# Kernel tuning notes

Hardware: AMD Instinct MI355X
Metric: run time of the kernel (lower is better)

## Reference

```python
import jax, jax.numpy as jnp
import numpy as np

H = 16
D_MODEL = 1024
D_K = D_MODEL // H
B, S = 2, 2048


def setup_inputs() -> dict:
    key = jax.random.key(0)
    ks = jax.random.split(key, 11)
    scale = 1.0 / np.sqrt(D_MODEL)
    inp = {
        "query": jax.random.normal(ks[0], (B, S, D_MODEL), jnp.float32),
        "key": jax.random.normal(ks[1], (B, S, D_MODEL), jnp.float32),
        "value": jax.random.normal(ks[2], (B, S, D_MODEL), jnp.float32),
        # four nn.Linear(d_model, d_model): Wq, Wk, Wv, Wo (torch convention: y = x @ W.T + b)
        "Wq": jax.random.uniform(ks[3], (D_MODEL, D_MODEL), jnp.float32, -scale, scale),
        "bq": jax.random.uniform(ks[4], (D_MODEL,), jnp.float32, -scale, scale),
        "Wk": jax.random.uniform(ks[5], (D_MODEL, D_MODEL), jnp.float32, -scale, scale),
        "bk": jax.random.uniform(ks[6], (D_MODEL,), jnp.float32, -scale, scale),
        "Wv": jax.random.uniform(ks[7], (D_MODEL, D_MODEL), jnp.float32, -scale, scale),
        "bv": jax.random.uniform(ks[8], (D_MODEL,), jnp.float32, -scale, scale),
        "Wo": jax.random.uniform(ks[9], (D_MODEL, D_MODEL), jnp.float32, -scale, scale),
        "bo": jax.random.uniform(ks[10], (D_MODEL,), jnp.float32, -scale, scale),
    }
    return inp


def _split_heads(x):
    # [B, S, D] -> [B, H, S, d_k]
    b, s, _ = x.shape
    return x.reshape(b, s, H, D_K).transpose(0, 2, 1, 3)


def reference(query, key, value, Wq, bq, Wk, bk, Wv, bv, Wo, bo):
    q = _split_heads(query @ Wq.T + bq)
    k = _split_heads(key @ Wk.T + bk)
    v = _split_heads(value @ Wv.T + bv)
    # scaled dot-product attention (dropout omitted: reference is eval-mode)
    scores = jnp.einsum("bhqd,bhkd->bhqk", q, k) / np.sqrt(D_K).astype(np.float32)
    p = jax.nn.softmax(scores, axis=-1)
    x = jnp.einsum("bhqk,bhkd->bhqd", p, v)
    x = x.transpose(0, 2, 1, 3).reshape(query.shape[0], -1, H * D_K)
    return x @ Wo.T + bo
```

## Files before the change

kernel.cpp:

```cpp
#include <hip/hip_runtime.h>

typedef unsigned short u16;
typedef unsigned int u32;
typedef __attribute__((ext_vector_type(8))) short short8;
typedef __attribute__((ext_vector_type(4))) float floatx4;
typedef __attribute__((ext_vector_type(4))) unsigned short ushortx4;
typedef __attribute__((ext_vector_type(4))) unsigned int uint4v;

#define DEV static __device__ __forceinline__

DEV float bf2f(u16 u) { union { unsigned u; float f; } v; v.u = ((unsigned)u) << 16; return v.f; }
DEV u16 f2bf(float f) {
  union { float f; unsigned u; } v; v.f = f;
  return (u16)((v.u + 0x7FFFu + ((v.u >> 16) & 1u)) >> 16);
}
DEV u32 pkbf(float a, float b) {
  union { float f; u32 u; } x, y; x.f = a; y.f = b;
  return __builtin_amdgcn_perm(y.u + 0x8000u, x.u + 0x8000u, 0x07060302u);
}
DEV float fexp2(float x) { return __builtin_amdgcn_exp2f(x); }

#define GLDS(g, l) __builtin_amdgcn_global_load_lds( \
    (const __attribute__((address_space(1))) void*)(g), \
    (__attribute__((address_space(3))) void*)(l), 16, 0, 0)

struct CvtArg {
  const float* src[11];
  u16* dst[11];
  int cum[12];
};

__global__ void convert(CvtArg a) {
  const long base = ((long)blockIdx.x * 256 + threadIdx.x) * 4;
  if (base >= a.cum[11]) return;
  int s = 0;
  while (s < 10 && base >= a.cum[s + 1]) ++s;
  const long off = base - a.cum[s];
  const float* sp = a.src[s] + off;
  ushortx4 u;
#pragma unroll
  for (int r = 0; r < 4; ++r) u[r] = f2bf(sp[r]);
  *(ushortx4*)(a.dst[s] + off) = u;
}

struct GemmArg {
  const u16* x;
  const u16* w;
  const u16* bias;
  u16* dst;
  int mode;
};

__global__ __launch_bounds__(256, 2) void gemm_nt(GemmArg g0, GemmArg g1, GemmArg g2) {
  GemmArg g = (blockIdx.z == 0) ? g0 : ((blockIdx.z == 1) ? g1 : g2);
  __shared__ u16 As[128 * 32];
  __shared__ u16 Bs[128 * 32];
  const int tid = threadIdx.x, w = tid >> 6, l = tid & 63;
  const int l15 = l & 15, quad = l >> 4;
  const int bm = blockIdx.x, bn = blockIdx.y;
  const int wm = w >> 1, wn = w & 1;

  floatx4 acc[4][4];
#pragma unroll
  for (int i = 0; i < 4; ++i)
#pragma unroll
    for (int j = 0; j < 4; ++j) acc[i][j] = (floatx4){0.f, 0.f, 0.f, 0.f};

  const u16* xb = g.x + (long)(bm * 128 + w * 16 + (l >> 2)) * 1024 + (l & 3) * 8;
  const u16* wb = g.w + (long)(bn * 128 + w * 16 + (l >> 2)) * 1024 + (l & 3) * 8;
  u16* asb = &As[(w * 16) * 32];
  u16* bsb = &Bs[(w * 16) * 32];

  for (int kt = 0; kt < 32; ++kt) {
    const int k0 = kt * 32;
    __syncthreads();
#pragma unroll
    for (int p = 0; p < 2; ++p) {
      GLDS(xb + (long)p * 64 * 1024 + k0, asb + p * 64 * 32);
      GLDS(wb + (long)p * 64 * 1024 + k0, bsb + p * 64 * 32);
    }
    __syncthreads();
    short8 af[4], bfr[4];
#pragma unroll
    for (int mi = 0; mi < 4; ++mi)
      af[mi] = *(const short8*)&As[(wm * 64 + mi * 16 + l15) * 32 + quad * 8];
#pragma unroll
    for (int ni = 0; ni < 4; ++ni)
      bfr[ni] = *(const short8*)&Bs[(wn * 64 + ni * 16 + l15) * 32 + quad * 8];
#pragma unroll
    for (int mi = 0; mi < 4; ++mi)
#pragma unroll
      for (int ni = 0; ni < 4; ++ni)
        acc[mi][ni] = __builtin_amdgcn_mfma_f32_16x16x32_bf16(af[mi], bfr[ni], acc[mi][ni], 0, 0, 0);
  }

  float bv[4];
#pragma unroll
  for (int ni = 0; ni < 4; ++ni) bv[ni] = bf2f(g.bias[bn * 128 + wn * 64 + ni * 16 + l15]);

#pragma unroll
  for (int mi = 0; mi < 4; ++mi) {
    const int mbase = bm * 128 + wm * 64 + mi * 16 + quad * 4;
#pragma unroll
    for (int ni = 0; ni < 4; ++ni) {
      const int n = bn * 128 + wn * 64 + ni * 16 + l15;
      if (g.mode == 2) {
        const int b = mbase >> 11, s = mbase & 2047;
        const int h = n >> 6, d = n & 63;
        ushortx4 u;
#pragma unroll
        for (int r = 0; r < 4; ++r) u[r] = f2bf(acc[mi][ni][r] + bv[ni]);
        *(ushortx4*)&g.dst[((long)(b * 16 + h) * 64 + d) * 2048 + s] = u;
      } else if (g.mode == 3) {
        float* df = (float*)g.dst;
#pragma unroll
        for (int r = 0; r < 4; ++r)
          df[(long)(mbase + r) * 1024 + n] = acc[mi][ni][r] + bv[ni];
      } else {
        const float sc = (g.mode == 0) ? 0.18033688011f : 1.0f;
        const int h = n >> 6, d = n & 63;
#pragma unroll
        for (int r = 0; r < 4; ++r) {
          const int m = mbase + r, b = m >> 11, s = m & 2047;
          g.dst[((long)(b * 16 + h) * 2048 + s) * 64 + d] = f2bf((acc[mi][ni][r] + bv[ni]) * sc);
        }
      }
    }
  }
}

__global__ __launch_bounds__(256, 2) void attn_flash(const u16* __restrict__ Q,
                                                     const u16* __restrict__ K,
                                                     const u16* __restrict__ V,
                                                     u16* __restrict__ X) {
  __shared__ u16 Ks[2][64 * 72];
  const int tid = threadIdx.x, w = tid >> 6, l = tid & 63;
  const int l15 = l & 15, quad = l >> 4;

  const int bid = blockIdx.x;
  const int xcd = bid & 7, idx = bid >> 3;
  const int qx = idx & 15, bh = xcd + 8 * (idx >> 4);
  const int q0 = qx * 128;

  const u16* qp = Q + (long)bh * 2048 * 64;
  const u16* kp = K + (long)bh * 2048 * 64;
  const u16* vp = V + (long)bh * 2048 * 64;

  const int r0 = tid >> 3, c0 = tid & 7, r1 = 32 + (tid >> 3);

#define ISSUE_K(kv0) \
    sk0 = *(const short8*)(kp + (long)((kv0) + r0) * 64 + c0 * 8); \
    sk1 = *(const short8*)(kp + (long)((kv0) + r1) * 64 + c0 * 8);

#define STORE_K(pb_) \
    *(short8*)&Ks[pb_][r0 * 72 + c0 * 8] = sk0; \
    *(short8*)&Ks[pb_][r1 * 72 + c0 * 8] = sk1;

  short8 sk0, sk1;

  short8 qf[2][2];
#pragma unroll
  for (int nq = 0; nq < 2; ++nq)
#pragma unroll
    for (int kc = 0; kc < 2; ++kc)
      qf[nq][kc] = *(const short8*)(qp + (long)(q0 + w * 32 + nq * 16 + l15) * 64 + kc * 32 + quad * 8);

  floatx4 o[2][4];
#pragma unroll
  for (int nq = 0; nq < 2; ++nq)
#pragma unroll
    for (int nd = 0; nd < 4; ++nd) o[nq][nd] = (floatx4){0.f, 0.f, 0.f, 0.f};
  float den[2] = {0.f, 0.f};

  const bool p1 = (l & 32) != 0;
  const bool p3 = (l & 16) != 0;
  const bool p2 = p1 ^ p3;

#define BFLY(pbv, m00, m01, m10, m11) { \
    u32 A0 = p1 ? (m10) : (m00), A1 = p1 ? (m11) : (m01); \
    u32 s0_ = p1 ? (m00) : (m10), s1_ = p1 ? (m01) : (m11); \
    u32 B0 = (u32)__shfl_xor((int)s0_, 32), B1 = (u32)__shfl_xor((int)s1_, 32); \
    u32 t0 = p2 ? A0 : B0, t1 = p2 ? A1 : B1; \
    u32 u0 = (u32)__shfl_xor((int)t0, 16), u1 = (u32)__shfl_xor((int)t1, 16); \
    u32 w0 = p2 ? B0 : A0, w1 = p2 ? B1 : A1; \
    pbv[0] = p3 ? u0 : w0; pbv[1] = p3 ? u1 : w1; \
    pbv[2] = p3 ? w0 : u0; pbv[3] = p3 ? w1 : u1; \
  }

  ISSUE_K(0)
  STORE_K(0)
  ISSUE_K(64)
  __syncthreads();

  for (int t = 0; t < 32; ++t) {
    const int p = t & 1;

    short8 vf[2][4];
#pragma unroll
    for (int kc = 0; kc < 2; ++kc)
#pragma unroll
      for (int nd = 0; nd < 4; ++nd)
        vf[kc][nd] = *(const short8*)(vp + (long)(nd * 16 + l15) * 2048 + (long)t * 64 + kc * 32 + quad * 8);

    u32 pk[2][4][2];
#pragma unroll
    for (int mk = 0; mk < 4; ++mk) {
      short8 ak0 = *(const short8*)&Ks[p][(mk * 16 + l15) * 72 + quad * 8];
      short8 ak1 = *(const short8*)&Ks[p][(mk * 16 + l15) * 72 + 32 + quad * 8];
#pragma unroll
      for (int nq = 0; nq < 2; ++nq) {
        floatx4 st = (floatx4){0.f, 0.f, 0.f, 0.f};
        st = __builtin_amdgcn_mfma_f32_16x16x32_bf16(ak0, qf[nq][0], st, 0, 0, 0);
        st = __builtin_amdgcn_mfma_f32_16x16x32_bf16(ak1, qf[nq][1], st, 0, 0, 0);
        const float e0 = fexp2(st[0]), e1 = fexp2(st[1]);
        const float e2 = fexp2(st[2]), e3 = fexp2(st[3]);
        den[nq] += (e0 + e1) + (e2 + e3);
        pk[nq][mk][0] = pkbf(e0, e1);
        pk[nq][mk][1] = pkbf(e2, e3);
      }
    }

#pragma unroll
    for (int kc = 0; kc < 2; ++kc) {
#pragma unroll
      for (int nq = 0; nq < 2; ++nq) {
        uint4v pb;
        BFLY(pb, pk[nq][2 * kc][0], pk[nq][2 * kc][1], pk[nq][2 * kc + 1][0], pk[nq][2 * kc + 1][1])
        short8 pbs = __builtin_bit_cast(short8, pb);
#pragma unroll
        for (int nd = 0; nd < 4; ++nd)
          o[nq][nd] = __builtin_amdgcn_mfma_f32_16x16x32_bf16(vf[kc][nd], pbs, o[nq][nd], 0, 0, 0);
      }
    }

    if (t < 31) {
      STORE_K(p ^ 1)
      if (t < 30) {
        ISSUE_K((t + 2) * 64)
      }
    }
    __syncthreads();
  }

  float rcp[2];
#pragma unroll
  for (int nq = 0; nq < 2; ++nq) {
    float d = den[nq];
    d += __shfl_xor(d, 16);
    d += __shfl_xor(d, 32);
    rcp[nq] = 1.0f / d;
  }

  const int b = bh >> 4, h = bh & 15;
#pragma unroll
  for (int nq = 0; nq < 2; ++nq) {
    const int s = q0 + w * 32 + nq * 16 + l15;
    u16* xrow = X + ((long)(b * 2048 + s)) * 1024 + h * 64;
#pragma unroll
    for (int nd = 0; nd < 4; ++nd) {
      ushortx4 u;
#pragma unroll
      for (int r = 0; r < 4; ++r) u[r] = f2bf(o[nq][nd][r] * rcp[nq]);
      *(ushortx4*)&xrow[nd * 16 + quad * 4] = u;
    }
  }
}

extern "C" void kernel_launch(void* const* d_in, const int* in_sizes, int n_in,
                              void* d_out, int out_size, void* d_ws, size_t ws_size,
                              hipStream_t stream) {
  u16* ws = (u16*)d_ws;
  const size_t M1 = 1048576, M4 = 4194304;
  u16* NQ  = ws;
  u16* NK  = ws + M4;
  u16* NV  = ws + 2 * M4;
  u16* NWQ = ws + 3 * M4;
  u16* NWK = ws + 3 * M4 + M1;
  u16* NWV = ws + 3 * M4 + 2 * M1;
  u16* NWO = ws + 3 * M4 + 3 * M1;
  u16* NBQ = ws + 3 * M4 + 4 * M1;
  u16* NBK = NBQ + 1024;
  u16* NBV = NBQ + 2048;
  u16* NBO = NBQ + 3072;
  u16* Qb = ws + 16 * M1 + 8192;
  u16* Kb = Qb + M4;
  u16* Vb = Qb + 2 * M4;
  u16* Xb = NQ;

  CvtArg ca;
  u16* dsts[11] = {NQ, NK, NV, NWQ, NBQ, NWK, NBK, NWV, NBV, NWO, NBO};
  int sizes[11] = {(int)M4, (int)M4, (int)M4, (int)M1, 1024, (int)M1, 1024, (int)M1, 1024, (int)M1, 1024};
  int c = 0;
  for (int i = 0; i < 11; ++i) {
    ca.src[i] = (const float*)d_in[i];
    ca.dst[i] = dsts[i];
    ca.cum[i] = c;
    c += sizes[i];
  }
  ca.cum[11] = c;
  convert<<<(c / 4 + 255) / 256, 256, 0, stream>>>(ca);

  GemmArg gq{NQ, NWQ, NBQ, Qb, 0};
  GemmArg gk{NK, NWK, NBK, Kb, 1};
  GemmArg gv{NV, NWV, NBV, Vb, 2};
  gemm_nt<<<dim3(32, 8, 3), 256, 0, stream>>>(gq, gk, gv);

  attn_flash<<<dim3(512), 256, 0, stream>>>(Qb, Kb, Vb, Xb);

  GemmArg go{Xb, NWO, NBO, (u16*)d_out, 3};
  gemm_nt<<<dim3(32, 8, 1), 256, 0, stream>>>(go, go, go);
}
```

Baseline: 244.3 us.

## Split KV tile across waves, stage V in LDS, use fp16 for PV

Flash attention now stages V tiles in shared memory alongside K with a double buffer, instead of each wave reading V directly from global memory. Work is re-partitioned so each wave handles 64 query rows against half of each 64-key tile. The two key-halves are merged at the end through shared memory. V and the probabilities switch to fp16 with a pack-with-truncation conversion and an f16 MFMA for the PV product. This is meant to cut redundant global V loads and the bf16 rounding overhead, at the cost of more registers per wave, an extra cross-wave reduction, and fp16 range and precision risk on V.

New measurement: 228.4 us. 1.07x faster.

```diff
diff --git a/kernel.cpp b/kernel.cpp
--- a/kernel.cpp
+++ b/kernel.cpp
@@ -3,6 +3,7 @@
 typedef unsigned short u16;
 typedef unsigned int u32;
 typedef __attribute__((ext_vector_type(8))) short short8;
+typedef __attribute__((ext_vector_type(8))) _Float16 half8;
 typedef __attribute__((ext_vector_type(4))) float floatx4;
 typedef __attribute__((ext_vector_type(4))) unsigned short ushortx4;
 typedef __attribute__((ext_vector_type(4))) unsigned int uint4v;
@@ -14,9 +15,9 @@
   union { float f; unsigned u; } v; v.f = f;
   return (u16)((v.u + 0x7FFFu + ((v.u >> 16) & 1u)) >> 16);
 }
-DEV u32 pkbf(float a, float b) {
-  union { float f; u32 u; } x, y; x.f = a; y.f = b;
-  return __builtin_amdgcn_perm(y.u + 0x8000u, x.u + 0x8000u, 0x07060302u);
+DEV u16 f2h(float f) { return __builtin_bit_cast(u16, (_Float16)f); }
+DEV u32 pkh(float a, float b) {
+  return __builtin_bit_cast(u32, __builtin_amdgcn_cvt_pkrtz(a, b));
 }
 DEV float fexp2(float x) { return __builtin_amdgcn_exp2f(x); }
 
@@ -109,7 +110,7 @@
         const int h = n >> 6, d = n & 63;
         ushortx4 u;
 #pragma unroll
-        for (int r = 0; r < 4; ++r) u[r] = f2bf(acc[mi][ni][r] + bv[ni]);
+        for (int r = 0; r < 4; ++r) u[r] = f2h(acc[mi][ni][r] + bv[ni]);
         *(ushortx4*)&g.dst[((long)(b * 16 + h) * 64 + d) * 2048 + s] = u;
       } else if (g.mode == 3) {
         float* df = (float*)g.dst;
@@ -133,9 +134,10 @@
                                                      const u16* __restrict__ K,
                                                      const u16* __restrict__ V,
                                                      u16* __restrict__ X) {
-  __shared__ u16 Ks[2][64 * 72];
+  __shared__ u16 KVs[4][64 * 72];
   const int tid = threadIdx.x, w = tid >> 6, l = tid & 63;
   const int l15 = l & 15, quad = l >> 4;
+  const int qh = w >> 1, kh = w & 1;
 
   const int bid = blockIdx.x;
   const int xcd = bid & 7, idx = bid >> 3;
@@ -148,29 +150,33 @@
 
   const int r0 = tid >> 3, c0 = tid & 7, r1 = 32 + (tid >> 3);
 
-#define ISSUE_K(kv0) \
+#define ISSUE_LOADS(kv0) \
     sk0 = *(const short8*)(kp + (long)((kv0) + r0) * 64 + c0 * 8); \
-    sk1 = *(const short8*)(kp + (long)((kv0) + r1) * 64 + c0 * 8);
-
-#define STORE_K(pb_) \
-    *(short8*)&Ks[pb_][r0 * 72 + c0 * 8] = sk0; \
-    *(short8*)&Ks[pb_][r1 * 72 + c0 * 8] = sk1;
-
-  short8 sk0, sk1;
-
-  short8 qf[2][2];
-#pragma unroll
-  for (int nq = 0; nq < 2; ++nq)
+    sv0 = *(const short8*)(vp + (long)r0 * 2048 + (kv0) + c0 * 8); \
+    sk1 = *(const short8*)(kp + (long)((kv0) + r1) * 64 + c0 * 8); \
+    sv1 = *(const short8*)(vp + (long)r1 * 2048 + (kv0) + c0 * 8);
+
+#define STORE_TILE(pb_) \
+    *(short8*)&KVs[pb_][r0 * 72 + c0 * 8] = sk0; \
+    *(short8*)&KVs[2 + (pb_)][r0 * 72 + c0 * 8] = sv0; \
+    *(short8*)&KVs[pb_][r1 * 72 + c0 * 8] = sk1; \
+    *(short8*)&KVs[2 + (pb_)][r1 * 72 + c0 * 8] = sv1;
+
+  short8 sk0, sv0, sk1, sv1;
+
+  short8 qf[4][2];
+#pragma unroll
+  for (int nq = 0; nq < 4; ++nq)
 #pragma unroll
     for (int kc = 0; kc < 2; ++kc)
-      qf[nq][kc] = *(const short8*)(qp + (long)(q0 + w * 32 + nq * 16 + l15) * 64 + kc * 32 + quad * 8);
-
-  floatx4 o[2][4];
-#pragma unroll
-  for (int nq = 0; nq < 2; ++nq)
+      qf[nq][kc] = *(const short8*)(qp + (long)(q0 + qh * 64 + nq * 16 + l15) * 64 + kc * 32 + quad * 8);
+
+  floatx4 o[4][4];
+#pragma unroll
+  for (int nq = 0; nq < 4; ++nq)
 #pragma unroll
     for (int nd = 0; nd < 4; ++nd) o[nq][nd] = (floatx4){0.f, 0.f, 0.f, 0.f};
-  float den[2] = {0.f, 0.f};
+  float den[4] = {0.f, 0.f, 0.f, 0.f};
 
   const bool p1 = (l & 32) != 0;
   const bool p3 = (l & 16) != 0;
@@ -187,81 +193,97 @@
     pbv[2] = p3 ? w0 : u0; pbv[3] = p3 ? w1 : u1; \
   }
 
-  ISSUE_K(0)
-  STORE_K(0)
-  ISSUE_K(64)
+  ISSUE_LOADS(0)
+  STORE_TILE(0)
+  ISSUE_LOADS(64)
   __syncthreads();
 
   for (int t = 0; t < 32; ++t) {
     const int p = t & 1;
 
-    short8 vf[2][4];
-#pragma unroll
-    for (int kc = 0; kc < 2; ++kc)
-#pragma unroll
-      for (int nd = 0; nd < 4; ++nd)
-        vf[kc][nd] = *(const short8*)(vp + (long)(nd * 16 + l15) * 2048 + (long)t * 64 + kc * 32 + quad * 8);
-
-    u32 pk[2][4][2];
-#pragma unroll
-    for (int mk = 0; mk < 4; ++mk) {
-      short8 ak0 = *(const short8*)&Ks[p][(mk * 16 + l15) * 72 + quad * 8];
-      short8 ak1 = *(const short8*)&Ks[p][(mk * 16 + l15) * 72 + 32 + quad * 8];
-#pragma unroll
-      for (int nq = 0; nq < 2; ++nq) {
+    u32 pk[4][2][2];
+#pragma unroll
+    for (int mk = 0; mk < 2; ++mk) {
+      const int krow = kh * 32 + mk * 16 + l15;
+      short8 ak0 = *(const short8*)&KVs[p][krow * 72 + quad * 8];
+      short8 ak1 = *(const short8*)&KVs[p][krow * 72 + 32 + quad * 8];
+#pragma unroll
+      for (int nq = 0; nq < 4; ++nq) {
         floatx4 st = (floatx4){0.f, 0.f, 0.f, 0.f};
         st = __builtin_amdgcn_mfma_f32_16x16x32_bf16(ak0, qf[nq][0], st, 0, 0, 0);
         st = __builtin_amdgcn_mfma_f32_16x16x32_bf16(ak1, qf[nq][1], st, 0, 0, 0);
         const float e0 = fexp2(st[0]), e1 = fexp2(st[1]);
         const float e2 = fexp2(st[2]), e3 = fexp2(st[3]);
         den[nq] += (e0 + e1) + (e2 + e3);
-        pk[nq][mk][0] = pkbf(e0, e1);
-        pk[nq][mk][1] = pkbf(e2, e3);
+        pk[nq][mk][0] = pkh(e0, e1);
+        pk[nq][mk][1] = pkh(e2, e3);
       }
     }
 
-#pragma unroll
-    for (int kc = 0; kc < 2; ++kc) {
-#pragma unroll
-      for (int nq = 0; nq < 2; ++nq) {
-        uint4v pb;
-        BFLY(pb, pk[nq][2 * kc][0], pk[nq][2 * kc][1], pk[nq][2 * kc + 1][0], pk[nq][2 * kc + 1][1])
-        short8 pbs = __builtin_bit_cast(short8, pb);
-#pragma unroll
-        for (int nd = 0; nd < 4; ++nd)
-          o[nq][nd] = __builtin_amdgcn_mfma_f32_16x16x32_bf16(vf[kc][nd], pbs, o[nq][nd], 0, 0, 0);
+    half8 vf[4];
+#pragma unroll
+    for (int nd = 0; nd < 4; ++nd)
+      vf[nd] = *(const half8*)&KVs[2 + p][(nd * 16 + l15) * 72 + kh * 32 + quad * 8];
+#pragma unroll
+    for (int nq = 0; nq < 4; ++nq) {
+      uint4v pb;
+      BFLY(pb, pk[nq][0][0], pk[nq][0][1], pk[nq][1][0], pk[nq][1][1])
+      half8 pbs = __builtin_bit_cast(half8, pb);
+#pragma unroll
+      for (int nd = 0; nd < 4; ++nd)
+        o[nq][nd] = __builtin_amdgcn_mfma_f32_16x16x32_f16(vf[nd], pbs, o[nq][nd], 0, 0, 0);
+    }
+
+    if (t < 31) {
+      STORE_TILE(p ^ 1)
+      if (t < 30) {
+        ISSUE_LOADS((t + 2) * 64)
       }
     }
-
-    if (t < 31) {
-      STORE_K(p ^ 1)
-      if (t < 30) {
-        ISSUE_K((t + 2) * 64)
-      }
-    }
     __syncthreads();
   }
 
-  float rcp[2];
-#pragma unroll
-  for (int nq = 0; nq < 2; ++nq) {
+  float dsum[4];
+#pragma unroll
+  for (int nq = 0; nq < 4; ++nq) {
     float d = den[nq];
     d += __shfl_xor(d, 16);
     d += __shfl_xor(d, 32);
-    rcp[nq] = 1.0f / d;
-  }
-
-  const int b = bh >> 4, h = bh & 15;
-#pragma unroll
-  for (int nq = 0; nq < 2; ++nq) {
-    const int s = q0 + w * 32 + nq * 16 + l15;
-    u16* xrow = X + ((long)(b * 2048 + s)) * 1024 + h * 64;
-#pragma unroll
-    for (int nd = 0; nd < 4; ++nd) {
-      ushortx4 u;
-#pragma unroll
-      for (int r = 0; r < 4; ++r) u[r] = f2bf(o[nq][nd][r] * rcp[nq]);
-      *(ushortx4*)&xrow[nd * 16 + quad * 4] = u;
+    dsum[nq] = d;
+  }
+
+  float* osc = (float*)KVs;
+  float* dsc = osc + 8192;
+  if (kh == 1) {
+#pragma unroll
+    for (int nq = 0; nq < 4; ++nq)
+#pragma unroll
+      for (int nd = 0; nd < 4; ++nd)
+        *(floatx4*)&osc[(((qh * 4 + nq) * 4 + nd) * 64 + l) * 4] = o[nq][nd];
+    if (l < 16) {
+#pragma unroll
+      for (int nq = 0; nq < 4; ++nq) dsc[(qh * 4 + nq) * 16 + l] = dsum[nq];
+    }
+  }
+  __syncthreads();
+
+  if (kh == 0) {
+    float rcp[4];
+#pragma unroll
+    for (int nq = 0; nq < 4; ++nq) rcp[nq] = 1.0f / (dsum[nq] + dsc[(qh * 4 + nq) * 16 + l15]);
+    const int b = bh >> 4, h = bh & 15;
+#pragma unroll
+    for (int nq = 0; nq < 4; ++nq) {
+      const int s = q0 + qh * 64 + nq * 16 + l15;
+      u16* xrow = X + ((long)(b * 2048 + s)) * 1024 + h * 64;
+#pragma unroll
+      for (int nd = 0; nd < 4; ++nd) {
+        floatx4 om = o[nq][nd] + *(const floatx4*)&osc[(((qh * 4 + nq) * 4 + nd) * 64 + l) * 4];
+        ushortx4 u;
+#pragma unroll
+        for (int r = 0; r < 4; ++r) u[r] = f2bf(om[r] * rcp[nq]);
+        *(ushortx4*)&xrow[nd * 16 + quad * 4] = u;
+      }
     }
   }
 }
```
